# Optimization experiments

Measured on AMD Instinct MI355X. Metric: run time of the kernel, lower is better.

Reference implementation:

```python
import jax, jax.numpy as jnp
import numpy as np

B, S, D, T, A, C, TB = 64, 256, 1024, 24, 128, 64, 16
NEG = -1e9


def setup_inputs() -> dict:
    key = jax.random.key(0)
    ks = jax.random.split(key, 24)
    sd = 1.0 / np.sqrt(D)
    s3 = 1.0 / np.sqrt(3 * D)
    inp = {
        'memory': jax.random.normal(ks[0], (B, S, D), jnp.float32),
        'encoded_col': jax.random.normal(ks[1], (B, C, D), jnp.float32),
        'encoded_tab': jax.random.normal(ks[2], (B, TB, D), jnp.float32),
        'init_h': jax.random.normal(ks[3], (B, D), jnp.float32),
        'init_c': jax.random.normal(ks[4], (B, D), jnp.float32),
        'prev_emb': jax.random.normal(ks[5], (T, B, D), jnp.float32),
        'node_emb': jax.random.normal(ks[6], (T, B, D), jnp.float32),
        'W_att': jax.random.normal(ks[7], (D, D), jnp.float32) * sd,
        'b_att': jnp.zeros((D,), jnp.float32),
        'W_tgt': jax.random.normal(ks[8], (D, D), jnp.float32) * sd,
        'b_tgt': jnp.zeros((D,), jnp.float32),
        'W_out': jax.random.normal(ks[9], (D, D), jnp.float32) * sd,
        'b_out': jnp.zeros((D,), jnp.float32),
        'W_ih': jax.random.normal(ks[10], (4 * D, 3 * D), jnp.float32) * s3,
        'W_hh': jax.random.normal(ks[11], (4 * D, D), jnp.float32) * sd,
        'b_ih': jnp.zeros((4 * D,), jnp.float32),
        'b_hh': jnp.zeros((4 * D,), jnp.float32),
        'action_emb': jax.random.normal(ks[12], (A, D), jnp.float32) * sd,
        'memory_mask': jnp.zeros((B, S), jnp.int32),
        'col_mask': jnp.zeros((B, C), jnp.int32),
        'tab_mask': jnp.zeros((B, TB), jnp.int32),
        'gold_action': jax.random.randint(ks[13], (T, B), 0, A, jnp.int32),
        'gold_col': jax.random.randint(ks[14], (T, B), 0, C, jnp.int32),
        'gold_tab': jax.random.randint(ks[15], (T, B), 0, TB, jnp.int32),
    }
    return inp


def reference(memory, encoded_col, encoded_tab, init_h, init_c, prev_emb, node_emb,
              W_att, b_att, W_tgt, b_tgt, W_out, b_out, W_ih, W_hh, b_ih, b_hh,
              action_emb, memory_mask, col_mask, tab_mask,
              gold_action, gold_col, gold_tab):
    # additive -inf biases where mask == 1 (masked)
    mem_bias = jnp.where(memory_mask == 1, NEG, 0.0)  # [B,S]
    col_bias = jnp.where(col_mask == 1, NEG, 0.0)      # [B,C]
    tab_bias = jnp.where(tab_mask == 1, NEG, 0.0)      # [B,TB]
    # att_affine_layer applied to the scoring sources (step-invariant -> hoist)
    act_src = action_emb @ W_att + b_att                # [A,D]
    col_src = jnp.einsum('bcd,de->bce', encoded_col, W_att) + b_att
    tab_src = jnp.einsum('btd,de->bte', encoded_tab, W_att) + b_att

    def step(carry, xs):
        h, c = carry
        prev_e, node_e, ga, gc, gt = xs
        # masked attention over memory, query = tgt_affine(h)
        q = h @ W_tgt + b_tgt                                      # [B,D]
        s = jnp.einsum('bsd,bd->bs', memory, q) + mem_bias          # [B,S]
        w = jax.nn.softmax(s, axis=-1)
        ctx = jnp.einsum('bs,bsd->bd', w, memory)                   # [B,D]
        # LSTMCell
        x = jnp.concatenate([prev_e, node_e, ctx], axis=-1)        # [B,3D]
        gates = x @ W_ih.T + h @ W_hh.T + b_ih + b_hh               # [B,4D]
        i, f, g, o = jnp.split(gates, 4, axis=-1)
        c_new = jax.nn.sigmoid(f) * c + jax.nn.sigmoid(i) * jnp.tanh(g)
        h_new = jax.nn.sigmoid(o) * jnp.tanh(c_new)
        out = h_new @ W_out + b_out                                 # [B,D]
        # grammar / column / table scoring heads (log-softmax probs)
        lp_a = jax.nn.log_softmax(jnp.einsum('ad,bd->ba', act_src, out), axis=-1)
        lp_c = jax.nn.log_softmax(jnp.einsum('bcd,bd->bc', col_src, out) + col_bias, axis=-1)
        lp_t = jax.nn.log_softmax(jnp.einsum('btd,bd->bt', tab_src, out) + tab_bias, axis=-1)
        ll = (jnp.take_along_axis(lp_a, ga[:, None], axis=1).sum()
              + jnp.take_along_axis(lp_c, gc[:, None], axis=1).sum()
              + jnp.take_along_axis(lp_t, gt[:, None], axis=1).sum())
        return (h_new, c_new), ll

    (_, _), lls = jax.lax.scan(step, (init_h, init_c),
                               (prev_emb, node_emb, gold_action, gold_col, gold_tab))
    loss = -jnp.sum(lls)
    return loss
```

## Files before the change

kernel.cpp:

```cpp
#include <hip/hip_runtime.h>
#include <math.h>

#define NEGB (-1e9f)
typedef float4 f4;

__device__ __forceinline__ float wsum(float v){
#pragma unroll
  for (int m = 32; m; m >>= 1) v += __shfl_xor(v, m, 64);
  return v;
}
__device__ __forceinline__ float wmaxr(float v){
#pragma unroll
  for (int m = 32; m; m >>= 1) v = fmaxf(v, __shfl_xor(v, m, 64));
  return v;
}
__device__ __forceinline__ f4 ld4(const float* p){ return *reinterpret_cast<const f4*>(p); }
__device__ __forceinline__ void st4(float* p, f4 v){ *reinterpret_cast<f4*>(p) = v; }
__device__ __forceinline__ float dot4(f4 a, f4 b){
  return a.x*b.x + a.y*b.y + a.z*b.z + a.w*b.w;
}
__device__ __forceinline__ float sigm(float x){ return 1.0f/(1.0f + __expf(-x)); }

#define FMA4(a, s, v) { (a).x += (s)*(v).x; (a).y += (s)*(v).y; (a).z += (s)*(v).z; (a).w += (s)*(v).w; }


__global__ __launch_bounds__(64) void k_init(float* __restrict__ loss){
  if (threadIdx.x == 0) *loss = 0.f;
}

__global__ __launch_bounds__(256) void k_transpose64(const float* __restrict__ in,
    float* __restrict__ out){
  __shared__ float t64[64][33];
  int tid = threadIdx.x;
  int k0 = blockIdx.x * 32;
  int b = tid >> 2, kk = (tid & 3) * 8;
  f4 v0 = ld4(in + (size_t)b*1024 + k0 + kk);
  f4 v1 = ld4(in + (size_t)b*1024 + k0 + kk + 4);
  t64[b][kk+0]=v0.x; t64[b][kk+1]=v0.y; t64[b][kk+2]=v0.z; t64[b][kk+3]=v0.w;
  t64[b][kk+4]=v1.x; t64[b][kk+5]=v1.y; t64[b][kk+6]=v1.z; t64[b][kk+7]=v1.w;
  __syncthreads();
  int b2 = tid & 63, kg = tid >> 6;
#pragma unroll
  for (int i=0;i<8;++i){
    int kk2 = kg*8 + i;
    out[(size_t)(k0+kk2)*64 + b2] = t64[b2][kk2];
  }
}

__global__ __launch_bounds__(256) void k_wctk2(const float* __restrict__ W_att,
    const float* __restrict__ W_out, float* __restrict__ WcTk){
  __shared__ float Al[16][68];
  __shared__ float Bl[16][68];
  int tid = threadIdx.x;
  int d0 = (blockIdx.x >> 4) * 64, ep0 = (blockIdx.x & 15) * 64;
  int srow = tid >> 2, skk = (tid & 3) * 4;
  int m0 = (tid >> 4) * 4, n0 = (tid & 15) * 4;
  f4 acc[4];
#pragma unroll
  for (int i=0;i<4;++i){ acc[i].x=0;acc[i].y=0;acc[i].z=0;acc[i].w=0; }
  f4 pa = ld4(W_out + (size_t)(d0+srow)*1024 + skk);
  f4 pb = ld4(W_att + (size_t)(ep0+srow)*1024 + skk);
  for (int kc = 0; kc < 1024; kc += 16){
#pragma unroll
    for (int j=0;j<4;++j){
      (&Al[skk][srow])[j*68] = (&pa.x)[j];
      (&Bl[skk][srow])[j*68] = (&pb.x)[j];
    }
    __syncthreads();
    if (kc + 16 < 1024){
      pa = ld4(W_out + (size_t)(d0+srow)*1024 + kc + 16 + skk);
      pb = ld4(W_att + (size_t)(ep0+srow)*1024 + kc + 16 + skk);
    }
#pragma unroll
    for (int k=0;k<16;++k){
      f4 a4 = ld4(&Al[k][m0]);
      f4 b4 = ld4(&Bl[k][n0]);
      FMA4(acc[0], a4.x, b4);
      FMA4(acc[1], a4.y, b4);
      FMA4(acc[2], a4.z, b4);
      FMA4(acc[3], a4.w, b4);
    }
    __syncthreads();
  }
#pragma unroll
  for (int i=0;i<4;++i)
    st4(WcTk + (size_t)(d0+m0+i)*1024 + ep0 + n0, acc[i]);
}

__global__ __launch_bounds__(256) void k_ubias2(const float* __restrict__ W_att,
    const float* __restrict__ b_out, float* __restrict__ ub){
  int w = threadIdx.x >> 6, lane = threadIdx.x & 63;
  int ep = blockIdx.x*4 + w;
  const float* arow = W_att + (size_t)ep*1024;
  float acc = 0.f;
#pragma unroll
  for (int i=0;i<4;++i)
    acc += dot4(ld4(arow + i*256 + lane*4), ld4(b_out + i*256 + lane*4));
  float s = wsum(acc);
  if (lane == 0) ub[ep] = s;
}


#define SKQ 8
__global__ __launch_bounds__(256) void k_qu_gemm(
    const float* __restrict__ hT, const float* __restrict__ W_tgt,
    const float* __restrict__ WcTk, float* __restrict__ part){
  __shared__ float Al[16][68];
  __shared__ float Xl[16][68];
  int tid = threadIdx.x;
  int rt = blockIdx.x >> 3, ks = blockIdx.x & 7;
  int n0g = rt*64;
  int kbeg = ks*128;
  int skk = tid >> 4, sn4 = (tid & 15) * 4;
  int m0 = (tid >> 4) * 4, n0 = (tid & 15) * 4;
  const float* Wsrc = (rt < 16) ? (W_tgt + n0g) : (WcTk + (n0g - 1024));
  f4 acc[4];
#pragma unroll
  for (int i=0;i<4;++i){ acc[i].x=0;acc[i].y=0;acc[i].z=0;acc[i].w=0; }
  f4 pa = ld4(Wsrc + (size_t)(kbeg+skk)*1024 + sn4);
  f4 px = ld4(hT + (size_t)(kbeg+skk)*64 + sn4);
  for (int kc = kbeg; kc < kbeg+128; kc += 16){
    st4(&Al[skk][sn4], pa);
    st4(&Xl[skk][sn4], px);
    __syncthreads();
    if (kc + 16 < kbeg+128){
      pa = ld4(Wsrc + (size_t)(kc+16+skk)*1024 + sn4);
      px = ld4(hT + (size_t)(kc+16+skk)*64 + sn4);
    }
#pragma unroll
    for (int k=0;k<16;++k){
      f4 a4 = ld4(&Al[k][m0]);
      f4 x4 = ld4(&Xl[k][n0]);
      FMA4(acc[0], a4.x, x4);
      FMA4(acc[1], a4.y, x4);
      FMA4(acc[2], a4.z, x4);
      FMA4(acc[3], a4.w, x4);
    }
    __syncthreads();
  }
#pragma unroll
  for (int i=0;i<4;++i)
    st4(part + ((size_t)ks*2048 + n0g + m0 + i)*64 + n0, acc[i]);
}

__global__ __launch_bounds__(256) void k_qu_reduce(const float* __restrict__ part,
    const float* __restrict__ b_tgt, const float* __restrict__ ub,
    float* __restrict__ q, float* __restrict__ u){
  int idx = blockIdx.x*256 + threadIdx.x;
  int b = idx & 63, n = idx >> 6;
  float s = 0.f;
#pragma unroll
  for (int ks=0; ks<SKQ; ++ks) s += part[((size_t)ks*2048 + n)*64 + b];
  if (n < 1024) q[(size_t)b*1024 + n] = s + b_tgt[n];
  else          u[(size_t)b*1024 + n - 1024] = s + ub[n - 1024];
}

__device__ __forceinline__ f4 gx_load(const float* prev_e, const float* node_e,
    const float* ctxT, const float* hT, int kc, int tid){
  int sel = kc >> 10;
  if (sel <= 1){
    const float* src = (sel==0) ? prev_e : node_e;
    int b = tid >> 2, kk = (tid & 3)*4;
    return ld4(src + (size_t)b*1024 + (kc & 1023) + kk);
  } else {
    const float* src = (sel==2) ? (ctxT + (size_t)(kc-2048)*64)
                                : (hT  + (size_t)(kc-3072)*64);
    int kk = tid >> 4, b4 = (tid & 15)*4;
    return ld4(src + (size_t)kk*64 + b4);
  }
}
__device__ __forceinline__ void gx_store(float Xl[16][68], f4 v, int kc, int tid){
  if ((kc >> 10) <= 1){
    int b = tid >> 2, kk = (tid & 3)*4;
    Xl[kk+0][b]=v.x; Xl[kk+1][b]=v.y; Xl[kk+2][b]=v.z; Xl[kk+3][b]=v.w;
  } else {
    int kk = tid >> 4, b4 = (tid & 15)*4;
    st4(&Xl[kk][b4], v);
  }
}
__device__ __forceinline__ void gw_load(const float* W_ih, const float* W_hh,
    int r, int kc, int c8, f4* w){
  const float* src = (kc < 3072) ? (W_ih + (size_t)r*3072 + kc + c8)
                                 : (W_hh + (size_t)r*1024 + (kc-3072) + c8);
  w[0] = ld4(src); w[1] = ld4(src + 4);
}

__global__ __launch_bounds__(256) void k_gates_gemm(
    const float* __restrict__ prev_e, const float* __restrict__ node_e,
    const float* __restrict__ ctxT, const float* __restrict__ hT,
    const float* __restrict__ W_ih, const float* __restrict__ W_hh,
    float* __restrict__ part, int sk){
  __shared__ float Wl[16][132];
  __shared__ float Xl[16][68];
  int tid = threadIdx.x;
  int rt = blockIdx.x / sk, ks = blockIdx.x - rt*sk;
  int r0 = rt*128;
  int kper = 4096/sk;
  int kbeg = ks*kper, kend = kbeg + kper;
  int srow = tid >> 1, c8 = (tid & 1)*8;
  int m0 = (tid >> 3)*4, n0 = (tid & 7)*8;
  f4 acc[4][2];
#pragma unroll
  for (int i=0;i<4;++i){
    acc[i][0].x=0;acc[i][0].y=0;acc[i][0].z=0;acc[i][0].w=0;
    acc[i][1].x=0;acc[i][1].y=0;acc[i][1].z=0;acc[i][1].w=0;
  }
  f4 pw[2];
  gw_load(W_ih, W_hh, r0+srow, kbeg, c8, pw);
  f4 px = gx_load(prev_e, node_e, ctxT, hT, kbeg, tid);
  for (int kc = kbeg; kc < kend; kc += 16){
#pragma unroll
    for (int j=0;j<4;++j){
      Wl[c8+j][srow]   = (&pw[0].x)[j];
      Wl[c8+4+j][srow] = (&pw[1].x)[j];
    }
    gx_store(Xl, px, kc, tid);
    __syncthreads();
    if (kc + 16 < kend){
      gw_load(W_ih, W_hh, r0+srow, kc+16, c8, pw);
      px = gx_load(prev_e, node_e, ctxT, hT, kc+16, tid);
    }
#pragma unroll
    for (int k=0;k<16;++k){
      f4 w4 = ld4(&Wl[k][m0]);
      f4 x0 = ld4(&Xl[k][n0]);
      f4 x1 = ld4(&Xl[k][n0+4]);
      FMA4(acc[0][0], w4.x, x0); FMA4(acc[0][1], w4.x, x1);
      FMA4(acc[1][0], w4.y, x0); FMA4(acc[1][1], w4.y, x1);
      FMA4(acc[2][0], w4.z, x0); FMA4(acc[2][1], w4.z, x1);
      FMA4(acc[3][0], w4.w, x0); FMA4(acc[3][1], w4.w, x1);
    }
    __syncthreads();
  }
#pragma unroll
  for (int i=0;i<4;++i){
    float* dst = part + ((size_t)ks*4096 + r0 + m0 + i)*64 + n0;
    st4(dst, acc[i][0]); st4(dst+4, acc[i][1]);
  }
}

__global__ __launch_bounds__(256) void k_lstm(const float* __restrict__ part,
    const float* __restrict__ b_ih, const float* __restrict__ b_hh,
    float* __restrict__ hT, float* __restrict__ cT, int sk){
  int idx = blockIdx.x*256 + threadIdx.x;
  int b = idx & 63, j = idx >> 6;
  float g[4];
#pragma unroll
  for (int gg=0; gg<4; ++gg){
    int r = gg*1024 + j;
    float s = b_ih[r] + b_hh[r];
    for (int ks=0; ks<sk; ++ks) s += part[((size_t)ks*4096 + r)*64 + b];
    g[gg] = s;
  }
  float c_old = cT[idx];
  float cn = sigm(g[1])*c_old + sigm(g[0])*tanhf(g[2]);
  float hn = sigm(g[3])*tanhf(cn);
  hT[idx] = hn;
  cT[idx] = cn;
}

__global__ __launch_bounds__(256) void k_attn_part(const float* __restrict__ memory,
    const float* __restrict__ q, const int* __restrict__ mmask,
    float* __restrict__ pa){
  __shared__ float cs[4][1024];
  __shared__ float mw[4], lw[4];
  int b = blockIdx.x >> 3, sc = blockIdx.x & 7;
  int w = threadIdx.x >> 6, lane = threadIdx.x & 63;
  const float* qb = q + (size_t)b*1024;
  f4 qf[4];
#pragma unroll
  for (int i=0;i<4;++i) qf[i] = ld4(qb + i*256 + lane*4);
  float m = -INFINITY, l = 0.f;
  f4 ca[4];
#pragma unroll
  for (int i=0;i<4;++i){ ca[i].x=0;ca[i].y=0;ca[i].z=0;ca[i].w=0; }
  for (int rr=0; rr<8; ++rr){
    int s = sc*32 + w*8 + rr;
    const float* mr = memory + ((size_t)b*256 + s)*1024;
    f4 a[4];
#pragma unroll
    for (int i=0;i<4;++i) a[i] = ld4(mr + i*256 + lane*4);
    float acc = 0.f;
#pragma unroll
    for (int i=0;i<4;++i) acc += dot4(a[i], qf[i]);
    float sv = wsum(acc) + (mmask[b*256+s]==1 ? NEGB : 0.f);
    float mn = fmaxf(m, sv);
    float al = __expf(m - mn);
    float p  = __expf(sv - mn);
    l = l*al + p;
#pragma unroll
    for (int i=0;i<4;++i){
      ca[i].x = ca[i].x*al + a[i].x*p;
      ca[i].y = ca[i].y*al + a[i].y*p;
      ca[i].z = ca[i].z*al + a[i].z*p;
      ca[i].w = ca[i].w*al + a[i].w*p;
    }
    m = mn;
  }
#pragma unroll
  for (int i=0;i<4;++i) st4(&cs[w][i*256 + lane*4], ca[i]);
  if (lane == 0){ mw[w] = m; lw[w] = l; }
  __syncthreads();
  int k4 = threadIdx.x*4;
  float M = fmaxf(fmaxf(mw[0],mw[1]), fmaxf(mw[2],mw[3]));
  float c0 = __expf(mw[0]-M), c1 = __expf(mw[1]-M);
  float c2 = __expf(mw[2]-M), c3 = __expf(mw[3]-M);
  float L = c0*lw[0] + c1*lw[1] + c2*lw[2] + c3*lw[3];
  f4 t0 = ld4(&cs[0][k4]), t1 = ld4(&cs[1][k4]);
  f4 t2 = ld4(&cs[2][k4]), t3 = ld4(&cs[3][k4]);
  f4 o;
  o.x = c0*t0.x + c1*t1.x + c2*t2.x + c3*t3.x;
  o.y = c0*t0.y + c1*t1.y + c2*t2.y + c3*t3.y;
  o.z = c0*t0.z + c1*t1.z + c2*t2.z + c3*t3.z;
  o.w = c0*t0.w + c1*t1.w + c2*t2.w + c3*t3.w;
  float* pb = pa + (size_t)(b*8+sc)*1040;
  st4(pb + k4, o);
  if (threadIdx.x == 0){ pb[1024] = M; pb[1025] = L; }
}

__global__ __launch_bounds__(256) void k_attn_merge(const float* __restrict__ pa,
    float* __restrict__ ctxT){
  int b = blockIdx.x;
  int tid = threadIdx.x;
  const float* pb = pa + (size_t)b*8*1040;
  float mm[8], ll[8];
#pragma unroll
  for (int s=0;s<8;++s){ mm[s] = pb[s*1040 + 1024]; ll[s] = pb[s*1040 + 1025]; }
  float M = mm[0];
#pragma unroll
  for (int s=1;s<8;++s) M = fmaxf(M, mm[s]);
  float co[8], L = 0.f;
#pragma unroll
  for (int s=0;s<8;++s){ co[s] = __expf(mm[s]-M); L += co[s]*ll[s]; }
  float inv = 1.f / L;
  int k4 = tid*4;
#pragma unroll
  for (int i=0;i<4;++i){
    int k = k4 + i;
    float v = 0.f;
#pragma unroll
    for (int s=0;s<8;++s) v += co[s]*pb[s*1040 + k];
    ctxT[(size_t)k*64 + b] = v * inv;
  }
}

__global__ __launch_bounds__(256) void k_scores(
    const float* __restrict__ u, const float* __restrict__ action_emb,
    const float* __restrict__ enc_col, const float* __restrict__ enc_tab,
    const int* __restrict__ col_mask, const int* __restrict__ tab_mask,
    const int* __restrict__ gold_a, const int* __restrict__ gold_c,
    const int* __restrict__ gold_t, int t, float* __restrict__ loss){
  __shared__ float s_all[208];
  __shared__ float hll[3];
  int b = blockIdx.x;
  int w = threadIdx.x >> 6, lane = threadIdx.x & 63;
  const float* ubp = u + (size_t)b*1024;
  f4 uf[4];
#pragma unroll
  for (int i=0;i<4;++i) uf[i] = ld4(ubp + i*256 + lane*4);
  for (int rr=0; rr<52; ++rr){
    int r = w*52 + rr;
    const float* src; float bias = 0.f;
    if (r < 128){
      src = action_emb + (size_t)r*1024;
    } else if (r < 192){
      int cc = r - 128;
      src = enc_col + ((size_t)b*64 + cc)*1024;
      bias = (col_mask[b*64+cc]==1) ? NEGB : 0.f;
    } else {
      int tt = r - 192;
      src = enc_tab + ((size_t)b*16 + tt)*1024;
      bias = (tab_mask[b*16+tt]==1) ? NEGB : 0.f;
    }
    float acc = 0.f;
#pragma unroll
    for (int i=0;i<4;++i) acc += dot4(ld4(src + i*256 + lane*4), uf[i]);
    float s = wsum(acc) + bias;
    if (lane == 0) s_all[r] = s;
  }
  __syncthreads();
  if (w == 0){
    float v0 = s_all[lane], v1 = s_all[64+lane];
    float M = wmaxr(fmaxf(v0, v1));
    float L = wsum(__expf(v0-M) + __expf(v1-M));
    if (lane == 0){ int g = gold_a[t*64+b]; hll[0] = s_all[g] - M - logf(L); }
  } else if (w == 1){
    float v = s_all[128+lane];
    float M = wmaxr(v);
    float L = wsum(__expf(v-M));
    if (lane == 0){ int g = gold_c[t*64+b]; hll[1] = s_all[128+g] - M - logf(L); }
  } else if (w == 2){
    float v = (lane < 16) ? s_all[192+lane] : -INFINITY;
    float M = wmaxr(v);
    float L = wsum((lane < 16) ? __expf(v-M) : 0.f);
    if (lane == 0){ int g = gold_t[t*64+b]; hll[2] = s_all[192+g] - M - logf(L); }
  }
  __syncthreads();
  if (threadIdx.x == 0) atomicAdd(loss, -(hll[0]+hll[1]+hll[2]));
}


extern "C" void kernel_launch(void* const* d_in, const int* in_sizes, int n_in,
                              void* d_out, int out_size, void* d_ws, size_t ws_size,
                              hipStream_t stream){
  const float* memory    = (const float*)d_in[0];
  const float* enc_col   = (const float*)d_in[1];
  const float* enc_tab   = (const float*)d_in[2];
  const float* init_h    = (const float*)d_in[3];
  const float* init_c    = (const float*)d_in[4];
  const float* prev_emb  = (const float*)d_in[5];
  const float* node_emb  = (const float*)d_in[6];
  const float* W_att     = (const float*)d_in[7];
  const float* W_tgt     = (const float*)d_in[9];
  const float* b_tgt     = (const float*)d_in[10];
  const float* W_out     = (const float*)d_in[11];
  const float* b_out     = (const float*)d_in[12];
  const float* W_ih      = (const float*)d_in[13];
  const float* W_hh      = (const float*)d_in[14];
  const float* b_ih      = (const float*)d_in[15];
  const float* b_hh      = (const float*)d_in[16];
  const float* action_emb= (const float*)d_in[17];
  const int*   mem_mask  = (const int*)d_in[18];
  const int*   col_mask  = (const int*)d_in[19];
  const int*   tab_mask  = (const int*)d_in[20];
  const int*   gold_a    = (const int*)d_in[21];
  const int*   gold_c    = (const int*)d_in[22];
  const int*   gold_t    = (const int*)d_in[23];

  float* ws   = (float*)d_ws;
  float* WcTk = ws;
  float* ub   = WcTk + 1048576;
  float* hT   = ub   + 1024;
  float* cT   = hT   + 65536;
  float* q    = cT   + 65536;
  float* u    = q    + 65536;
  float* ctxT = u    + 65536;
  float* pa   = ctxT + 65536;
  float* part = pa   + 532480;
  float* loss = (float*)d_out;

  size_t fixedf = 1048576 + 1024 + (size_t)5*65536 + 532480;
  size_t availf = (ws_size/4 > fixedf) ? (ws_size/4 - fixedf) : 0;
  int skg = 16;
  if (availf < (size_t)16*4096*64) skg = 8;
  if (availf < (size_t)8*4096*64)  skg = 4;

  k_init       <<<1,   64, 0, stream>>>(loss);
  k_transpose64<<<32, 256, 0, stream>>>(init_h, hT);
  k_transpose64<<<32, 256, 0, stream>>>(init_c, cT);
  k_wctk2      <<<256,256, 0, stream>>>(W_att, W_out, WcTk);
  k_ubias2     <<<256,256, 0, stream>>>(W_att, b_out, ub);
  k_qu_gemm    <<<32*SKQ,256,0,stream>>>(hT, W_tgt, WcTk, part);
  k_qu_reduce  <<<512,256, 0, stream>>>(part, b_tgt, ub, q, u);

  for (int t = 0; t < 24; ++t){
    k_attn_part <<<512, 256, 0, stream>>>(memory, q, mem_mask, pa);
    k_attn_merge<<<64,  256, 0, stream>>>(pa, ctxT);
    k_gates_gemm<<<32*skg,256,0, stream>>>(prev_emb + (size_t)t*65536,
                                           node_emb + (size_t)t*65536,
                                           ctxT, hT, W_ih, W_hh, part, skg);
    k_lstm      <<<256, 256, 0, stream>>>(part, b_ih, b_hh, hT, cT, skg);
    k_qu_gemm   <<<32*SKQ,256,0,stream>>>(hT, W_tgt, WcTk, part);
    k_qu_reduce <<<512, 256, 0, stream>>>(part, b_tgt, ub, q, u);
    k_scores    <<<64,  256, 0, stream>>>(u, action_emb, enc_col, enc_tab,
                                          col_mask, tab_mask, gold_a, gold_c, gold_t,
                                          t, loss);
  }
}
```

Baseline: 3.156 ms.

## Restructure scoring kernel into smem-tiled, register-prefetched dot products

Replaces the per-row wavefront-reduction scoring kernel with a version that stages 208x64 chunks of the score sources into padded shared memory. Loads are register-prefetched one chunk ahead so global reads overlap compute. Each thread then computes one full row dot product serially, which removes the 52 sequential wave shuffle reductions per wave. The costs are large shared-memory use, 32 barriers per block, and 48 idle threads during compute, with still only 64 blocks launched.

```diff
diff --git a/kernel.cpp b/kernel.cpp
--- a/kernel.cpp
+++ b/kernel.cpp
@@ -344,41 +344,59 @@
   }
 }
 
-__global__ __launch_bounds__(256) void k_scores(
+__global__ __launch_bounds__(256) void k_scores2(
     const float* __restrict__ u, const float* __restrict__ action_emb,
     const float* __restrict__ enc_col, const float* __restrict__ enc_tab,
     const int* __restrict__ col_mask, const int* __restrict__ tab_mask,
     const int* __restrict__ gold_a, const int* __restrict__ gold_c,
     const int* __restrict__ gold_t, int t, float* __restrict__ loss){
+  __shared__ float Es[208][65];
+  __shared__ float us[1024];
   __shared__ float s_all[208];
   __shared__ float hll[3];
-  int b = blockIdx.x;
-  int w = threadIdx.x >> 6, lane = threadIdx.x & 63;
-  const float* ubp = u + (size_t)b*1024;
-  f4 uf[4];
-#pragma unroll
-  for (int i=0;i<4;++i) uf[i] = ld4(ubp + i*256 + lane*4);
-  for (int rr=0; rr<52; ++rr){
-    int r = w*52 + rr;
-    const float* src; float bias = 0.f;
-    if (r < 128){
-      src = action_emb + (size_t)r*1024;
-    } else if (r < 192){
-      int cc = r - 128;
-      src = enc_col + ((size_t)b*64 + cc)*1024;
-      bias = (col_mask[b*64+cc]==1) ? NEGB : 0.f;
-    } else {
-      int tt = r - 192;
-      src = enc_tab + ((size_t)b*16 + tt)*1024;
-      bias = (tab_mask[b*16+tt]==1) ? NEGB : 0.f;
-    }
-    float acc = 0.f;
-#pragma unroll
-    for (int i=0;i<4;++i) acc += dot4(ld4(src + i*256 + lane*4), uf[i]);
-    float s = wsum(acc) + bias;
-    if (lane == 0) s_all[r] = s;
+  int b = blockIdx.x, tid = threadIdx.x;
+  st4(&us[tid*4], ld4(u + (size_t)b*1024 + tid*4));
+  float acc = 0.f;
+  f4 pv[13];
+#define SC_LOAD(c) {                                                         \
+    _Pragma("unroll")                                                        \
+    for (int i=0;i<13;++i){                                                  \
+      int idx = i*256 + tid;                                                 \
+      int row = idx >> 4, kk2 = (idx & 15)*4;                                \
+      int k = (c)*64 + kk2;                                                  \
+      const float* src;                                                      \
+      if (row < 128)      src = action_emb + (size_t)row*1024 + k;           \
+      else if (row < 192) src = enc_col + ((size_t)b*64 + (row-128))*1024 + k;\
+      else                src = enc_tab + ((size_t)b*16 + (row-192))*1024 + k;\
+      pv[i] = ld4(src);                                                      \
+    } }
+  SC_LOAD(0);
+  for (int c = 0; c < 16; ++c){
+#pragma unroll
+    for (int i=0;i<13;++i){
+      int idx = i*256 + tid;
+      int row = idx >> 4, kk2 = (idx & 15)*4;
+      Es[row][kk2+0] = pv[i].x; Es[row][kk2+1] = pv[i].y;
+      Es[row][kk2+2] = pv[i].z; Es[row][kk2+3] = pv[i].w;
+    }
+    __syncthreads();
+    if (c + 1 < 16) SC_LOAD(c + 1);
+    if (tid < 208){
+#pragma unroll
+      for (int j=0;j<64;++j)
+        acc += Es[tid][j] * us[c*64 + j];
+    }
+    __syncthreads();
+  }
+#undef SC_LOAD
+  if (tid < 208){
+    float bias = 0.f;
+    if (tid >= 192)      bias = (tab_mask[b*16 + (tid-192)]==1) ? NEGB : 0.f;
+    else if (tid >= 128) bias = (col_mask[b*64 + (tid-128)]==1) ? NEGB : 0.f;
+    s_all[tid] = acc + bias;
   }
   __syncthreads();
+  int w = tid >> 6, lane = tid & 63;
   if (w == 0){
     float v0 = s_all[lane], v1 = s_all[64+lane];
     float M = wmaxr(fmaxf(v0, v1));
@@ -396,7 +414,7 @@
     if (lane == 0){ int g = gold_t[t*64+b]; hll[2] = s_all[192+g] - M - logf(L); }
   }
   __syncthreads();
-  if (threadIdx.x == 0) atomicAdd(loss, -(hll[0]+hll[1]+hll[2]));
+  if (tid == 0) atomicAdd(loss, -(hll[0]+hll[1]+hll[2]));
 }
 
 
@@ -462,7 +480,7 @@
     k_lstm      <<<256, 256, 0, stream>>>(part, b_ih, b_hh, hT, cT, skg);
     k_qu_gemm   <<<32*SKQ,256,0,stream>>>(hT, W_tgt, WcTk, part);
     k_qu_reduce <<<512, 256, 0, stream>>>(part, b_tgt, ub, q, u);
-    k_scores    <<<64,  256, 0, stream>>>(u, action_emb, enc_col, enc_tab,
+    k_scores2   <<<64,  256, 0, stream>>>(u, action_emb, enc_col, enc_tab,
                                           col_mask, tab_mask, gold_a, gold_c, gold_t,
                                           t, loss);
   }
```

Result: faster. 2.775 ms (-12.1%).
